# Optimization experiments

Measured on AMD Instinct MI355X. Metric: run time of the kernel, lower is better.

## Reference

```python
import jax, jax.numpy as jnp
import numpy as np


def setup_inputs() -> dict:
    key = jax.random.key(0)
    k1, k2, k3, k4, k5 = jax.random.split(key, 5)
    B, C, H, W = 2, 3, 64, 64
    f_tar = jax.random.normal(k1, (B, C, H, W), dtype=jnp.float32)
    f_src = jax.random.normal(k2, (B, C, H, W), dtype=jnp.float32)
    # Pinhole intrinsics (focal=50, principal point at image center) + small noise,
    # guaranteed invertible.
    K_base = jnp.array([[50.0, 0.0, 32.0], [0.0, 50.0, 32.0], [0.0, 0.0, 1.0]],
                       dtype=jnp.float32)
    K = K_base[None] + 0.05 * jax.random.normal(k3, (B, 3, 3), dtype=jnp.float32)
    # Near-identity rotation-like matrix.
    R = jnp.eye(3, dtype=jnp.float32)[None] + 0.1 * jax.random.normal(
        k4, (B, 3, 3), dtype=jnp.float32)
    t = jax.random.normal(k5, (B, 3, 1), dtype=jnp.float32)
    return {"f_tar": f_tar, "f_src": f_src, "K": K, "R": R, "t": t}


def reference(f_tar, f_src, K, R, t):
    B, C, H, W = f_src.shape  # C == 3 (required by the cross product)
    N = H * W
    dtype = f_src.dtype

    f_src_flat = f_src.reshape(B, C, N)  # (B, 3, N)
    f_tar_flat = f_tar.reshape(B, C, N)  # (B, 3, N)

    # A[b, i, j] = <f_src[:, i], f_tar[:, j]>  -> (B, N, N)
    A = jnp.einsum('bci,bcj->bij', f_src_flat, f_tar_flat)

    # Homogeneous pixel coordinates (3, N): rows of meshgrid(H, W, indexing='ij').
    ix, iy = jnp.meshgrid(jnp.arange(H), jnp.arange(W), indexing='ij')
    pix = jnp.stack([ix.reshape(-1), iy.reshape(-1), jnp.ones(N, dtype=jnp.int32)],
                    axis=0).astype(dtype)  # (3, N)

    K_inv = jnp.linalg.inv(K)  # (B, 3, 3)
    # tar_proj = K @ (R @ (K^-1 @ x) + t)   -> (B, 3, N)
    cam_rays = jnp.einsum('bij,jn->bin', K_inv, pix)
    tar_proj = jnp.einsum('bij,bjn->bin', K, jnp.einsum('bij,bjn->bin', R, cam_rays) + t)
    # Origin projects to K @ (R @ 0 + t) = K @ t, broadcast over N.
    o_proj = jnp.einsum('bij,bjn->bin', K, t)  # (B, 3, 1)

    diff = tar_proj - o_proj  # (B, 3, N)

    # Epipolar distance: || (f_src - o) x diff || / ||diff||, broadcast to (B, N, N).
    a = f_src_flat[:, :, :, None] - o_proj[:, :, :, None]  # (B, 3, N, 1)
    b = diff[:, :, None, :]                                 # (B, 3, 1, N)
    cross = jnp.cross(a, b, axis=1)                         # (B, 3, N, N)
    cross_norm = jnp.linalg.norm(cross, axis=1)             # (B, N, N)
    diff_norm = jnp.linalg.norm(diff, axis=1, keepdims=True)  # (B, 1, N)
    d_epipolar = cross_norm / diff_norm                     # (B, N, N)

    # 'sigmoid' in the original is nn.Softmax(dim=-1).
    EPI_THRESH = 0.5
    SHARPNESS = 50.0
    weight_map = 1.0 - jax.nn.softmax(SHARPNESS * (d_epipolar - EPI_THRESH), axis=-1)

    A_weighted = A * weight_map
    attention_map = jax.nn.softmax(A_weighted, axis=1)  # normalize over src positions

    # (B, N, N) @ (B, N, C) -> (B, N, C), then raw view back to (B, C, H, W)
    attended = jnp.einsum('bik,bck->bic', attention_map, f_src_flat)
    return attended.reshape(B, C, H, W)
```

## Files before the change

kernel.cpp:

```cpp
#include <hip/hip_runtime.h>

namespace {
constexpr int BB = 2;
constexpr int NN = 4096;
constexpr float LOG2E = 1.44269504088896340736f;
constexpr float T50 = 72.1347520444481703f;

constexpr int OFF_W4   = 0;
constexpr int OFF_IREC = 4 * BB * NN;
constexpr int OFF_JREC = 16 * BB * NN;
constexpr int OFF_NMAX = 28 * BB * NN;
}

__device__ __forceinline__ float fsqrt(float x) { return __builtin_amdgcn_sqrtf(x); }
__device__ __forceinline__ float fexp2(float x) {
#if __has_builtin(__builtin_amdgcn_exp2f)
  return __builtin_amdgcn_exp2f(x);
#else
  return __expf(x * 0.69314718055994530942f);
#endif
}

__global__ __launch_bounds__(256) void k_setup(
    const float* __restrict__ fsrc, const float* __restrict__ ftar,
    const float* __restrict__ Kb, const float* __restrict__ Rb,
    const float* __restrict__ tb, float* __restrict__ ws) {
  int gid = blockIdx.x * blockDim.x + threadIdx.x;
  if (gid >= BB * NN) return;
  int b = gid >> 12;
  int n = gid & (NN - 1);

  float K[9], R[9], t3[3];
#pragma unroll
  for (int k = 0; k < 9; k++) { K[k] = Kb[b * 9 + k]; R[k] = Rb[b * 9 + k]; }
#pragma unroll
  for (int k = 0; k < 3; k++) t3[k] = tb[b * 3 + k];

  float c00 = K[4] * K[8] - K[5] * K[7];
  float c01 = K[5] * K[6] - K[3] * K[8];
  float c02 = K[3] * K[7] - K[4] * K[6];
  float det = K[0] * c00 + K[1] * c01 + K[2] * c02;
  float id = 1.0f / det;
  float Ki[9];
  Ki[0] = c00 * id; Ki[1] = (K[2] * K[7] - K[1] * K[8]) * id; Ki[2] = (K[1] * K[5] - K[2] * K[4]) * id;
  Ki[3] = c01 * id; Ki[4] = (K[0] * K[8] - K[2] * K[6]) * id; Ki[5] = (K[2] * K[3] - K[0] * K[5]) * id;
  Ki[6] = c02 * id; Ki[7] = (K[1] * K[6] - K[0] * K[7]) * id; Ki[8] = (K[0] * K[4] - K[1] * K[3]) * id;

  float RK[9];
#pragma unroll
  for (int i = 0; i < 3; i++)
#pragma unroll
    for (int j = 0; j < 3; j++)
      RK[i * 3 + j] = R[i * 3 + 0] * Ki[j] + R[i * 3 + 1] * Ki[3 + j] + R[i * 3 + 2] * Ki[6 + j];
  float M3[9];
#pragma unroll
  for (int i = 0; i < 3; i++)
#pragma unroll
    for (int j = 0; j < 3; j++)
      M3[i * 3 + j] = K[i * 3 + 0] * RK[j] + K[i * 3 + 1] * RK[3 + j] + K[i * 3 + 2] * RK[6 + j];
  float o0 = K[0] * t3[0] + K[1] * t3[1] + K[2] * t3[2];
  float o1 = K[3] * t3[0] + K[4] * t3[1] + K[5] * t3[2];
  float o2 = K[6] * t3[0] + K[7] * t3[1] + K[8] * t3[2];

  float sx = fsrc[b * 3 * NN + 0 * NN + n];
  float sy = fsrc[b * 3 * NN + 1 * NN + n];
  float sz = fsrc[b * 3 * NN + 2 * NN + n];
  float tx = ftar[b * 3 * NN + 0 * NN + n];
  float ty = ftar[b * 3 * NN + 1 * NN + n];
  float tz = ftar[b * 3 * NN + 2 * NN + n];

  float ux = sx - o0, uy = sy - o1, uz = sz - o2;
  float usq = ux * ux + uy * uy + uz * uz;

  float px = (float)(n >> 6), py = (float)(n & 63);
  float vx = M3[0] * px + M3[1] * py + M3[2];
  float vy = M3[3] * px + M3[4] * py + M3[5];
  float vz = M3[6] * px + M3[7] * py + M3[8];
  float invn = rsqrtf(vx * vx + vy * vy + vz * vz);
  float wx = vx * invn, wy = vy * invn, wz = vz * invn;
  float tn = fsqrt(tx * tx + ty * ty + tz * tz);

  float4* w4 = (float4*)(ws + OFF_W4);
  float4* irec = (float4*)(ws + OFF_IREC);
  float4* jrec = (float4*)(ws + OFF_JREC);
  w4[gid] = make_float4(wx, wy, wz, 0.f);
  irec[gid * 3 + 0] = make_float4(ux, uy, uz, usq);
  irec[gid * 3 + 1] = make_float4(sx, sy, sz, 0.f);
  jrec[gid * 3 + 0] = make_float4(wx, wy, wz, tn);
  jrec[gid * 3 + 1] = make_float4(tx, ty, tz, 0.f);
  jrec[gid * 3 + 2] = make_float4(sx, sy, sz, 0.f);

  float ns = fsqrt(sx * sx + sy * sy + sz * sz);
#pragma unroll
  for (int off = 32; off; off >>= 1) ns = fmaxf(ns, __shfl_xor(ns, off));
  if ((threadIdx.x & 63) == 0)
    atomicMax((unsigned int*)(ws + OFF_NMAX + b), __float_as_uint(ns));
}

__global__ __launch_bounds__(256, 4) void k_pass1(float* __restrict__ ws) {
  __shared__ float sred[4][8];
  __shared__ float smax[8];
  const float4* irec = (const float4*)(ws + OFF_IREC);
  int tid = threadIdx.x, wid = tid >> 6, lane = tid & 63;
  int g0 = blockIdx.x * 8;
  int b = g0 >> 12;
  const float4* wb = (const float4*)(ws + OFF_W4) + b * NN;

  float ux[8], uy[8], uz[8], us[8];
#pragma unroll
  for (int r = 0; r < 8; r++) {
    float4 u = irec[(g0 + r) * 3];
    ux[r] = u.x; uy[r] = u.y; uz[r] = u.z; us[r] = u.w;
  }

  float mx[8] = {0.f, 0.f, 0.f, 0.f, 0.f, 0.f, 0.f, 0.f};
  for (int j = wid * 64 + lane; j < NN; j += 256) {
    float4 w = wb[j];
#pragma unroll
    for (int r = 0; r < 8; r++) {
      float dot = ux[r] * w.x + uy[r] * w.y + uz[r] * w.z;
      mx[r] = fmaxf(mx[r], __builtin_fmaf(-dot, dot, us[r]));
    }
  }
#pragma unroll
  for (int off = 32; off; off >>= 1)
#pragma unroll
    for (int r = 0; r < 8; r++) mx[r] = fmaxf(mx[r], __shfl_xor(mx[r], off));
  if (lane == 0) {
#pragma unroll
    for (int r = 0; r < 8; r++) sred[wid][r] = mx[r];
  }
  __syncthreads();
  if (tid < 8)
    smax[tid] = T50 * fsqrt(fmaxf(fmaxf(sred[0][tid], sred[1][tid]),
                                  fmaxf(sred[2][tid], sred[3][tid])));
  __syncthreads();
  float m[8];
#pragma unroll
  for (int r = 0; r < 8; r++) m[r] = smax[r];

  float s[8] = {0.f, 0.f, 0.f, 0.f, 0.f, 0.f, 0.f, 0.f};
  for (int j = wid * 64 + lane; j < NN; j += 256) {
    float4 w = wb[j];
#pragma unroll
    for (int r = 0; r < 8; r++) {
      float dot = ux[r] * w.x + uy[r] * w.y + uz[r] * w.z;
      float d2 = fmaxf(__builtin_fmaf(-dot, dot, us[r]), 0.f);
      s[r] += fexp2(__builtin_fmaf(T50, fsqrt(d2), -m[r]));
    }
  }
#pragma unroll
  for (int off = 32; off; off >>= 1)
#pragma unroll
    for (int r = 0; r < 8; r++) s[r] += __shfl_xor(s[r], off);
  if (lane == 0) {
#pragma unroll
    for (int r = 0; r < 8; r++) sred[wid][r] = s[r];
  }
  __syncthreads();
  if (tid < 8) {
    float tot = sred[0][tid] + sred[1][tid] + sred[2][tid] + sred[3][tid];
    ws[OFF_IREC + (g0 + tid) * 12 + 7] = smax[tid];
    ws[OFF_IREC + (g0 + tid) * 12 + 8] = 1.f / tot;
  }
}

__global__ __launch_bounds__(256, 4) void k_pass2(float* __restrict__ ws) {
  __shared__ float sred[4][8];
  const float4* irec = (const float4*)(ws + OFF_IREC);
  const float4* jrec = (const float4*)(ws + OFF_JREC);
  int tid = threadIdx.x, wid = tid >> 6, lane = tid & 63;
  int c0 = blockIdx.x * 8;
  int b = c0 >> 12;
  int base = b * NN;
  float maxns2 = ws[OFF_NMAX + b] * LOG2E;

  float wx[8], wy[8], wz[8], tx2[8], ty2[8], tz2[8], Mb2[8];
#pragma unroll
  for (int r = 0; r < 8; r++) {
    float4 q0 = jrec[(c0 + r) * 3 + 0];
    float4 q1 = jrec[(c0 + r) * 3 + 1];
    wx[r] = q0.x; wy[r] = q0.y; wz[r] = q0.z;
    Mb2[r] = maxns2 * q0.w;
    tx2[r] = q1.x * LOG2E; ty2[r] = q1.y * LOG2E; tz2[r] = q1.z * LOG2E;
  }

  float S[8] = {0.f, 0.f, 0.f, 0.f, 0.f, 0.f, 0.f, 0.f};
  for (int i = wid * 64 + lane; i < NN; i += 256) {
    int idx = base + i;
    float4 u = irec[idx * 3 + 0];
    float4 sq = irec[idx * 3 + 1];
    float invden = ws[OFF_IREC + idx * 12 + 8];
#pragma unroll
    for (int r = 0; r < 8; r++) {
      float dot = u.x * wx[r] + u.y * wy[r] + u.z * wz[r];
      float d2 = fmaxf(__builtin_fmaf(-dot, dot, u.w), 0.f);
      float e = fexp2(__builtin_fmaf(T50, fsqrt(d2), -sq.w));
      float wgt = __builtin_fmaf(-e, invden, 1.f);
      float A2 = sq.x * tx2[r] + sq.y * ty2[r] + sq.z * tz2[r];
      S[r] += fexp2(__builtin_fmaf(A2, wgt, -Mb2[r]));
    }
  }
#pragma unroll
  for (int off = 32; off; off >>= 1)
#pragma unroll
    for (int r = 0; r < 8; r++) S[r] += __shfl_xor(S[r], off);
  if (lane == 0) {
#pragma unroll
    for (int r = 0; r < 8; r++) sred[wid][r] = S[r];
  }
  __syncthreads();
  if (tid < 8) {
    float tot = sred[0][tid] + sred[1][tid] + sred[2][tid] + sred[3][tid];
    float tn = jrec[(c0 + tid) * 3 + 0].w;
    ws[OFF_JREC + (c0 + tid) * 12 + 7] = maxns2 * tn;
    ws[OFF_JREC + (c0 + tid) * 12 + 11] = 1.f / tot;
  }
}

__global__ __launch_bounds__(256, 4) void k_pass3(const float* __restrict__ ws,
                                                  float* __restrict__ out) {
  __shared__ float sacc[4][24];
  const float4* irec = (const float4*)(ws + OFF_IREC);
  const float4* jrec = (const float4*)(ws + OFF_JREC);
  int tid = threadIdx.x, wid = tid >> 6, lane = tid & 63;
  int g0 = blockIdx.x * 8;
  int b = g0 >> 12;
  int base = b * NN;

  float ux[8], uy[8], uz[8], us[8], ml[8], inv[8], sx2[8], sy2[8], sz2[8];
#pragma unroll
  for (int r = 0; r < 8; r++) {
    float4 u = irec[(g0 + r) * 3 + 0];
    float4 sq = irec[(g0 + r) * 3 + 1];
    ux[r] = u.x; uy[r] = u.y; uz[r] = u.z; us[r] = u.w;
    sx2[r] = sq.x * LOG2E; sy2[r] = sq.y * LOG2E; sz2[r] = sq.z * LOG2E;
    ml[r] = sq.w;
    inv[r] = ws[OFF_IREC + (g0 + r) * 12 + 8];
  }
  float acc[8][3];
#pragma unroll
  for (int r = 0; r < 8; r++) { acc[r][0] = 0.f; acc[r][1] = 0.f; acc[r][2] = 0.f; }

  for (int j = wid * 64 + lane; j < NN; j += 256) {
    int idx = base + j;
    float4 q0 = jrec[idx * 3 + 0];
    float4 q1 = jrec[idx * 3 + 1];
    float4 q2 = jrec[idx * 3 + 2];
#pragma unroll
    for (int r = 0; r < 8; r++) {
      float dot = ux[r] * q0.x + uy[r] * q0.y + uz[r] * q0.z;
      float d2 = fmaxf(__builtin_fmaf(-dot, dot, us[r]), 0.f);
      float e = fexp2(__builtin_fmaf(T50, fsqrt(d2), -ml[r]));
      float wgt = __builtin_fmaf(-e, inv[r], 1.f);
      float A2 = sx2[r] * q1.x + sy2[r] * q1.y + sz2[r] * q1.z;
      float p = fexp2(__builtin_fmaf(A2, wgt, -q1.w)) * q2.w;
      acc[r][0] = __builtin_fmaf(p, q2.x, acc[r][0]);
      acc[r][1] = __builtin_fmaf(p, q2.y, acc[r][1]);
      acc[r][2] = __builtin_fmaf(p, q2.z, acc[r][2]);
    }
  }
#pragma unroll
  for (int off = 32; off; off >>= 1)
#pragma unroll
    for (int r = 0; r < 8; r++) {
      acc[r][0] += __shfl_xor(acc[r][0], off);
      acc[r][1] += __shfl_xor(acc[r][1], off);
      acc[r][2] += __shfl_xor(acc[r][2], off);
    }
  if (lane == 0) {
#pragma unroll
    for (int r = 0; r < 8; r++) {
      sacc[wid][r * 3 + 0] = acc[r][0];
      sacc[wid][r * 3 + 1] = acc[r][1];
      sacc[wid][r * 3 + 2] = acc[r][2];
    }
  }
  __syncthreads();
  if (tid < 24) {
    float v = sacc[0][tid] + sacc[1][tid] + sacc[2][tid] + sacc[3][tid];
    out[g0 * 3 + tid] = v;
  }
}

extern "C" void kernel_launch(void* const* d_in, const int* in_sizes, int n_in,
                              void* d_out, int out_size, void* d_ws, size_t ws_size,
                              hipStream_t stream) {
  (void)in_sizes; (void)n_in; (void)out_size; (void)ws_size;
  const float* ftar = (const float*)d_in[0];
  const float* fsrc = (const float*)d_in[1];
  const float* K = (const float*)d_in[2];
  const float* R = (const float*)d_in[3];
  const float* t = (const float*)d_in[4];
  float* ws = (float*)d_ws;
  float* out = (float*)d_out;

  hipMemsetAsync((char*)d_ws + OFF_NMAX * sizeof(float), 0, BB * sizeof(float), stream);

  k_setup<<<dim3((BB * NN + 255) / 256), dim3(256), 0, stream>>>(fsrc, ftar, K, R, t, ws);
  k_pass1<<<dim3(1024), dim3(256), 0, stream>>>(ws);
  k_pass2<<<dim3(1024), dim3(256), 0, stream>>>(ws);
  k_pass3<<<dim3(1024), dim3(256), 0, stream>>>(ws, out);
}
```

Before: 132.4 us.

## Fuse all passes into one cooperative kernel and fold softmax constants

```diff
diff --git a/kernel.cpp b/kernel.cpp
--- a/kernel.cpp
+++ b/kernel.cpp
@@ -1,15 +1,19 @@
 #include <hip/hip_runtime.h>
+#include <hip/hip_cooperative_groups.h>
+
+namespace cg = cooperative_groups;
 
 namespace {
 constexpr int BB = 2;
 constexpr int NN = 4096;
 constexpr float LOG2E = 1.44269504088896340736f;
 constexpr float T50 = 72.1347520444481703f;
+constexpr float T50SQ = T50 * T50;
 
 constexpr int OFF_W4   = 0;
 constexpr int OFF_IREC = 4 * BB * NN;
-constexpr int OFF_JREC = 16 * BB * NN;
-constexpr int OFF_NMAX = 28 * BB * NN;
+constexpr int OFF_JREC = 12 * BB * NN;
+constexpr int OFF_NMAX = 24 * BB * NN;
 }
 
 __device__ __forceinline__ float fsqrt(float x) { return __builtin_amdgcn_sqrtf(x); }
@@ -17,16 +21,21 @@
 #if __has_builtin(__builtin_amdgcn_exp2f)
   return __builtin_amdgcn_exp2f(x);
 #else
-  return __expf(x * 0.69314718055994530942f);
+  return exp2f(x);
 #endif
 }
-
-__global__ __launch_bounds__(256) void k_setup(
+__device__ __forceinline__ float flog2(float x) {
+#if __has_builtin(__builtin_amdgcn_logf)
+  return __builtin_amdgcn_logf(x);
+#else
+  return log2f(x);
+#endif
+}
+
+__device__ __forceinline__ void d_setup(int gid,
     const float* __restrict__ fsrc, const float* __restrict__ ftar,
     const float* __restrict__ Kb, const float* __restrict__ Rb,
     const float* __restrict__ tb, float* __restrict__ ws) {
-  int gid = blockIdx.x * blockDim.x + threadIdx.x;
-  if (gid >= BB * NN) return;
   int b = gid >> 12;
   int n = gid & (NN - 1);
 
@@ -76,7 +85,7 @@
   float vx = M3[0] * px + M3[1] * py + M3[2];
   float vy = M3[3] * px + M3[4] * py + M3[5];
   float vz = M3[6] * px + M3[7] * py + M3[8];
-  float invn = rsqrtf(vx * vx + vy * vy + vz * vz);
+  float invn = rsqrtf(vx * vx + vy * vy + vz * vz) * T50;
   float wx = vx * invn, wy = vy * invn, wz = vz * invn;
   float tn = fsqrt(tx * tx + ty * ty + tz * tz);
 
@@ -84,8 +93,8 @@
   float4* irec = (float4*)(ws + OFF_IREC);
   float4* jrec = (float4*)(ws + OFF_JREC);
   w4[gid] = make_float4(wx, wy, wz, 0.f);
-  irec[gid * 3 + 0] = make_float4(ux, uy, uz, usq);
-  irec[gid * 3 + 1] = make_float4(sx, sy, sz, 0.f);
+  irec[gid * 2 + 0] = make_float4(ux, uy, uz, usq * T50SQ);
+  irec[gid * 2 + 1] = make_float4(sx * LOG2E, sy * LOG2E, sz * LOG2E, 0.f);
   jrec[gid * 3 + 0] = make_float4(wx, wy, wz, tn);
   jrec[gid * 3 + 1] = make_float4(tx, ty, tz, 0.f);
   jrec[gid * 3 + 2] = make_float4(sx, sy, sz, 0.f);
@@ -97,19 +106,18 @@
     atomicMax((unsigned int*)(ws + OFF_NMAX + b), __float_as_uint(ns));
 }
 
-__global__ __launch_bounds__(256, 4) void k_pass1(float* __restrict__ ws) {
-  __shared__ float sred[4][8];
-  __shared__ float smax[8];
+__device__ __forceinline__ void d_pass1(int bid, int tid, float* __restrict__ ws,
+                                        float (*sred)[8], float* smax) {
   const float4* irec = (const float4*)(ws + OFF_IREC);
-  int tid = threadIdx.x, wid = tid >> 6, lane = tid & 63;
-  int g0 = blockIdx.x * 8;
+  int wid = tid >> 6, lane = tid & 63;
+  int g0 = bid * 8;
   int b = g0 >> 12;
   const float4* wb = (const float4*)(ws + OFF_W4) + b * NN;
 
   float ux[8], uy[8], uz[8], us[8];
 #pragma unroll
   for (int r = 0; r < 8; r++) {
-    float4 u = irec[(g0 + r) * 3];
+    float4 u = irec[(g0 + r) * 2];
     ux[r] = u.x; uy[r] = u.y; uz[r] = u.z; us[r] = u.w;
   }
 
@@ -132,8 +140,8 @@
   }
   __syncthreads();
   if (tid < 8)
-    smax[tid] = T50 * fsqrt(fmaxf(fmaxf(sred[0][tid], sred[1][tid]),
-                                  fmaxf(sred[2][tid], sred[3][tid])));
+    smax[tid] = fsqrt(fmaxf(fmaxf(fmaxf(sred[0][tid], sred[1][tid]),
+                                  fmaxf(sred[2][tid], sred[3][tid])), 0.f));
   __syncthreads();
   float m[8];
 #pragma unroll
@@ -146,7 +154,7 @@
     for (int r = 0; r < 8; r++) {
       float dot = ux[r] * w.x + uy[r] * w.y + uz[r] * w.z;
       float d2 = fmaxf(__builtin_fmaf(-dot, dot, us[r]), 0.f);
-      s[r] += fexp2(__builtin_fmaf(T50, fsqrt(d2), -m[r]));
+      s[r] += fexp2(fsqrt(d2) - m[r]);
     }
   }
 #pragma unroll
@@ -160,44 +168,42 @@
   __syncthreads();
   if (tid < 8) {
     float tot = sred[0][tid] + sred[1][tid] + sred[2][tid] + sred[3][tid];
-    ws[OFF_IREC + (g0 + tid) * 12 + 7] = smax[tid];
-    ws[OFF_IREC + (g0 + tid) * 12 + 8] = 1.f / tot;
-  }
-}
-
-__global__ __launch_bounds__(256, 4) void k_pass2(float* __restrict__ ws) {
-  __shared__ float sred[4][8];
+    ws[OFF_IREC + (g0 + tid) * 8 + 7] = smax[tid] + flog2(tot);
+  }
+}
+
+__device__ __forceinline__ void d_pass2(int bid, int tid, float* __restrict__ ws,
+                                        float (*sred)[8]) {
   const float4* irec = (const float4*)(ws + OFF_IREC);
   const float4* jrec = (const float4*)(ws + OFF_JREC);
-  int tid = threadIdx.x, wid = tid >> 6, lane = tid & 63;
-  int c0 = blockIdx.x * 8;
+  int wid = tid >> 6, lane = tid & 63;
+  int c0 = bid * 8;
   int b = c0 >> 12;
   int base = b * NN;
   float maxns2 = ws[OFF_NMAX + b] * LOG2E;
 
-  float wx[8], wy[8], wz[8], tx2[8], ty2[8], tz2[8], Mb2[8];
+  float wx[8], wy[8], wz[8], tx[8], ty[8], tz[8], Mb2[8];
 #pragma unroll
   for (int r = 0; r < 8; r++) {
     float4 q0 = jrec[(c0 + r) * 3 + 0];
     float4 q1 = jrec[(c0 + r) * 3 + 1];
     wx[r] = q0.x; wy[r] = q0.y; wz[r] = q0.z;
     Mb2[r] = maxns2 * q0.w;
-    tx2[r] = q1.x * LOG2E; ty2[r] = q1.y * LOG2E; tz2[r] = q1.z * LOG2E;
+    tx[r] = q1.x; ty[r] = q1.y; tz[r] = q1.z;
   }
 
   float S[8] = {0.f, 0.f, 0.f, 0.f, 0.f, 0.f, 0.f, 0.f};
   for (int i = wid * 64 + lane; i < NN; i += 256) {
     int idx = base + i;
-    float4 u = irec[idx * 3 + 0];
-    float4 sq = irec[idx * 3 + 1];
-    float invden = ws[OFF_IREC + idx * 12 + 8];
+    float4 u = irec[idx * 2 + 0];
+    float4 sq = irec[idx * 2 + 1];
 #pragma unroll
     for (int r = 0; r < 8; r++) {
       float dot = u.x * wx[r] + u.y * wy[r] + u.z * wz[r];
       float d2 = fmaxf(__builtin_fmaf(-dot, dot, u.w), 0.f);
-      float e = fexp2(__builtin_fmaf(T50, fsqrt(d2), -sq.w));
-      float wgt = __builtin_fmaf(-e, invden, 1.f);
-      float A2 = sq.x * tx2[r] + sq.y * ty2[r] + sq.z * tz2[r];
+      float en = fexp2(fsqrt(d2) - sq.w);
+      float wgt = 1.f - en;
+      float A2 = sq.x * tx[r] + sq.y * ty[r] + sq.z * tz[r];
       S[r] += fexp2(__builtin_fmaf(A2, wgt, -Mb2[r]));
     }
   }
@@ -212,31 +218,27 @@
   __syncthreads();
   if (tid < 8) {
     float tot = sred[0][tid] + sred[1][tid] + sred[2][tid] + sred[3][tid];
-    float tn = jrec[(c0 + tid) * 3 + 0].w;
-    ws[OFF_JREC + (c0 + tid) * 12 + 7] = maxns2 * tn;
-    ws[OFF_JREC + (c0 + tid) * 12 + 11] = 1.f / tot;
-  }
-}
-
-__global__ __launch_bounds__(256, 4) void k_pass3(const float* __restrict__ ws,
-                                                  float* __restrict__ out) {
-  __shared__ float sacc[4][24];
+    float Mb2t = maxns2 * jrec[(c0 + tid) * 3 + 0].w;
+    ws[OFF_JREC + (c0 + tid) * 12 + 7] = Mb2t + flog2(tot);
+  }
+}
+
+__device__ __forceinline__ void d_pass3(int bid, int tid, const float* __restrict__ ws,
+                                        float* __restrict__ out, float (*sacc)[24]) {
   const float4* irec = (const float4*)(ws + OFF_IREC);
   const float4* jrec = (const float4*)(ws + OFF_JREC);
-  int tid = threadIdx.x, wid = tid >> 6, lane = tid & 63;
-  int g0 = blockIdx.x * 8;
+  int wid = tid >> 6, lane = tid & 63;
+  int g0 = bid * 8;
   int b = g0 >> 12;
   int base = b * NN;
 
-  float ux[8], uy[8], uz[8], us[8], ml[8], inv[8], sx2[8], sy2[8], sz2[8];
+  float ux[8], uy[8], uz[8], us[8], ml[8], s2x[8], s2y[8], s2z[8];
 #pragma unroll
   for (int r = 0; r < 8; r++) {
-    float4 u = irec[(g0 + r) * 3 + 0];
-    float4 sq = irec[(g0 + r) * 3 + 1];
+    float4 u = irec[(g0 + r) * 2 + 0];
+    float4 sq = irec[(g0 + r) * 2 + 1];
     ux[r] = u.x; uy[r] = u.y; uz[r] = u.z; us[r] = u.w;
-    sx2[r] = sq.x * LOG2E; sy2[r] = sq.y * LOG2E; sz2[r] = sq.z * LOG2E;
-    ml[r] = sq.w;
-    inv[r] = ws[OFF_IREC + (g0 + r) * 12 + 8];
+    s2x[r] = sq.x; s2y[r] = sq.y; s2z[r] = sq.z; ml[r] = sq.w;
   }
   float acc[8][3];
 #pragma unroll
@@ -251,10 +253,10 @@
     for (int r = 0; r < 8; r++) {
       float dot = ux[r] * q0.x + uy[r] * q0.y + uz[r] * q0.z;
       float d2 = fmaxf(__builtin_fmaf(-dot, dot, us[r]), 0.f);
-      float e = fexp2(__builtin_fmaf(T50, fsqrt(d2), -ml[r]));
-      float wgt = __builtin_fmaf(-e, inv[r], 1.f);
-      float A2 = sx2[r] * q1.x + sy2[r] * q1.y + sz2[r] * q1.z;
-      float p = fexp2(__builtin_fmaf(A2, wgt, -q1.w)) * q2.w;
+      float en = fexp2(fsqrt(d2) - ml[r]);
+      float wgt = 1.f - en;
+      float A2 = s2x[r] * q1.x + s2y[r] * q1.y + s2z[r] * q1.z;
+      float p = fexp2(__builtin_fmaf(A2, wgt, -q1.w));
       acc[r][0] = __builtin_fmaf(p, q2.x, acc[r][0]);
       acc[r][1] = __builtin_fmaf(p, q2.y, acc[r][1]);
       acc[r][2] = __builtin_fmaf(p, q2.z, acc[r][2]);
@@ -281,6 +283,48 @@
     float v = sacc[0][tid] + sacc[1][tid] + sacc[2][tid] + sacc[3][tid];
     out[g0 * 3 + tid] = v;
   }
+}
+
+__global__ __launch_bounds__(256, 4) void k_fused(
+    const float* __restrict__ fsrc, const float* __restrict__ ftar,
+    const float* __restrict__ Kb, const float* __restrict__ Rb,
+    const float* __restrict__ tb, float* __restrict__ ws, float* __restrict__ out) {
+  cg::grid_group grid = cg::this_grid();
+  __shared__ float sred[4][8];
+  __shared__ float smax[8];
+  __shared__ float sacc[4][24];
+  int tid = threadIdx.x, bid = blockIdx.x;
+
+  int gid = bid * 256 + tid;
+  if (gid < BB * NN) d_setup(gid, fsrc, ftar, Kb, Rb, tb, ws);
+  grid.sync();
+  d_pass1(bid, tid, ws, sred, smax);
+  grid.sync();
+  d_pass2(bid, tid, ws, sred);
+  grid.sync();
+  d_pass3(bid, tid, ws, out, sacc);
+}
+
+__global__ __launch_bounds__(256) void k_setup_s(
+    const float* __restrict__ fsrc, const float* __restrict__ ftar,
+    const float* __restrict__ Kb, const float* __restrict__ Rb,
+    const float* __restrict__ tb, float* __restrict__ ws) {
+  int gid = blockIdx.x * 256 + threadIdx.x;
+  if (gid < BB * NN) d_setup(gid, fsrc, ftar, Kb, Rb, tb, ws);
+}
+__global__ __launch_bounds__(256, 4) void k_p1(float* __restrict__ ws) {
+  __shared__ float sred[4][8];
+  __shared__ float smax[8];
+  d_pass1(blockIdx.x, threadIdx.x, ws, sred, smax);
+}
+__global__ __launch_bounds__(256, 4) void k_p2(float* __restrict__ ws) {
+  __shared__ float sred[4][8];
+  d_pass2(blockIdx.x, threadIdx.x, ws, sred);
+}
+__global__ __launch_bounds__(256, 4) void k_p3(const float* __restrict__ ws,
+                                               float* __restrict__ out) {
+  __shared__ float sacc[4][24];
+  d_pass3(blockIdx.x, threadIdx.x, ws, out, sacc);
 }
 
 extern "C" void kernel_launch(void* const* d_in, const int* in_sizes, int n_in,
@@ -297,8 +341,14 @@
 
   hipMemsetAsync((char*)d_ws + OFF_NMAX * sizeof(float), 0, BB * sizeof(float), stream);
 
-  k_setup<<<dim3((BB * NN + 255) / 256), dim3(256), 0, stream>>>(fsrc, ftar, K, R, t, ws);
-  k_pass1<<<dim3(1024), dim3(256), 0, stream>>>(ws);
-  k_pass2<<<dim3(1024), dim3(256), 0, stream>>>(ws);
-  k_pass3<<<dim3(1024), dim3(256), 0, stream>>>(ws, out);
-}
+  void* args[] = {(void*)&fsrc, (void*)&ftar, (void*)&K, (void*)&R, (void*)&t,
+                  (void*)&ws, (void*)&out};
+  hipError_t err = hipLaunchCooperativeKernel((const void*)k_fused, dim3(1024),
+                                              dim3(256), args, 0, stream);
+  if (err != hipSuccess) {
+    k_setup_s<<<dim3(32), dim3(256), 0, stream>>>(fsrc, ftar, K, R, t, ws);
+    k_p1<<<dim3(1024), dim3(256), 0, stream>>>(ws);
+    k_p2<<<dim3(1024), dim3(256), 0, stream>>>(ws);
+    k_p3<<<dim3(1024), dim3(256), 0, stream>>>(ws, out);
+  }
+}
```

After: 462.9 us. +249.6%, slower.
